# Kernel tuning notes

Hardware: AMD Instinct MI355X
Metric: run time of the kernel (lower is better)

Reference implementation:

```python
import jax, jax.numpy as jnp
import numpy as np

FP8_MAX = 448.0  # float8_e4m3fn max
NUM_HEADS = 16

def _fp8_quant_dequant(t):
    # per-(batch, head) symmetric scaling into fp8 e4m3 range, cast to fp8 and back
    amax = jnp.max(jnp.abs(t), axis=(-2, -1), keepdims=True)
    scale = FP8_MAX / jnp.maximum(amax, 1e-12)
    t8 = (t * scale).astype(jnp.float8_e4m3fn).astype(t.dtype)
    return t8 / scale

def setup_inputs() -> dict:
    key = jax.random.key(0)
    k1, k2, k3 = jax.random.split(key, 3)
    B, N, C = 2, 2048, 1024
    x = jax.random.normal(k1, (B, N, C), dtype=jnp.float32)
    w_qkv = jax.random.normal(k2, (C, 3 * C), dtype=jnp.float32) * (C ** -0.5)
    w_proj = jax.random.normal(k3, (C, C), dtype=jnp.float32) * (C ** -0.5)
    b_proj = jnp.zeros((C,), dtype=jnp.float32)
    return {"x": x, "w_qkv": w_qkv, "w_proj": w_proj, "b_proj": b_proj}

def reference(x, w_qkv, w_proj, b_proj):
    B, N, C = x.shape
    H = NUM_HEADS
    D = C // H
    scale = D ** -0.5
    qkv = (x @ w_qkv).reshape(B, N, 3, H, D).transpose(2, 0, 3, 1, 4)  # [3,B,H,N,D]
    q, k, v = qkv[0], qkv[1], qkv[2]
    # sage-style fp8 quantize/dequant of q and k fused into score computation
    q = _fp8_quant_dequant(q)
    k = _fp8_quant_dequant(k)
    scores = jnp.einsum('bhqd,bhkd->bhqk', q, k) * scale  # [B,H,N,N]
    causal = jnp.tril(jnp.ones((N, N), dtype=bool))
    scores = jnp.where(causal[None, None], scores, jnp.finfo(scores.dtype).min)
    attn = jax.nn.softmax(scores, axis=-1)
    out = jnp.einsum('bhqk,bhkd->bhqd', attn, v)  # [B,H,N,D]
    out = out.transpose(0, 2, 1, 3).reshape(B, N, C)
    return out @ w_proj + b_proj
```

## Files before the change

### kernel.cpp

```cpp
#include <hip/hip_runtime.h>

#define B_   2
#define N_   2048
#define C_   1024
#define H_   16
#define D_   64
#define BH_  (B_*H_)
#define NDH  (N_*D_)
#define M1   (B_*N_)

typedef __attribute__((ext_vector_type(4))) float    f32x4;
typedef __attribute__((ext_vector_type(8))) _Float16 f16x8;
typedef __attribute__((ext_vector_type(4))) _Float16 f16x4;
typedef __attribute__((ext_vector_type(2))) __fp16   h16x2;

#define GLOAD_LDS(gp, lp) \
  __builtin_amdgcn_global_load_lds((const __attribute__((address_space(1))) void*)(gp), \
                                   (__attribute__((address_space(3))) void*)(lp), 16, 0, 0)

__global__ void k_cvt16(const float* __restrict__ in, _Float16* __restrict__ out, int n4) {
  int i = blockIdx.x * blockDim.x + threadIdx.x;
  if (i >= n4) return;
  float4 v = ((const float4*)in)[i];
  f16x4 o;
  o.x = (_Float16)v.x; o.y = (_Float16)v.y; o.z = (_Float16)v.z; o.w = (_Float16)v.w;
  ((f16x4*)out)[i] = o;
}

__global__ __launch_bounds__(256) void k_transmerge(const float* __restrict__ wq,
                                                    const float* __restrict__ wp,
                                                    _Float16* __restrict__ whT,
                                                    _Float16* __restrict__ wpT,
                                                    unsigned* __restrict__ amax_u) {
  if (blockIdx.x == 0 && threadIdx.x < 64) amax_u[threadIdx.x] = 0u;
  __shared__ _Float16 t[64][68];
  int idx = blockIdx.x;
  const float* in; _Float16* out; int Cc, cx, cy;
  if (idx < 768) { in = wq; out = whT; Cc = 3072; cx = idx % 48; cy = idx / 48; }
  else { idx -= 768; in = wp; out = wpT; Cc = 1024; cx = idx % 16; cy = idx / 16; }
  const int R = 1024;
  int c0 = cx * 64, r0 = cy * 64;
  int tid = threadIdx.x;
  int cq = tid & 15, rq = tid >> 4;
#pragma unroll
  for (int i = 0; i < 4; ++i) {
    int r = rq + i * 16;
    float4 v = *(const float4*)(in + (size_t)(r0 + r) * Cc + c0 + cq * 4);
    t[r][cq*4+0] = (_Float16)v.x;
    t[r][cq*4+1] = (_Float16)v.y;
    t[r][cq*4+2] = (_Float16)v.z;
    t[r][cq*4+3] = (_Float16)v.w;
  }
  __syncthreads();
#pragma unroll
  for (int i = 0; i < 4; ++i) {
    int c = rq + i * 16;
    f16x4 o;
    o.x = t[cq*4+0][c];
    o.y = t[cq*4+1][c];
    o.z = t[cq*4+2][c];
    o.w = t[cq*4+3][c];
    *(f16x4*)(out + (size_t)(c0 + c) * R + r0 + cq * 4) = o;
  }
}

__global__ __launch_bounds__(256) void k_gemm_qkv(const _Float16* __restrict__ A,
                                                  const _Float16* __restrict__ BT,
                                                  _Float16* __restrict__ qh,
                                                  _Float16* __restrict__ kh,
                                                  _Float16* __restrict__ vh,
                                                  unsigned* __restrict__ amax_u) {
  __shared__ __align__(16) _Float16 As[128 * 32];
  __shared__ __align__(16) _Float16 Bs[128 * 32];
  const int tid = threadIdx.x, lane = tid & 63, wave = tid >> 6;
  const int wm = wave >> 1, wn = wave & 1;
  const int mcol = lane & 15, quad = lane >> 4;
  const int m0 = blockIdx.x * 128, n0 = blockIdx.y * 128;
  f32x4 acc[4][4] = {};
  for (int k0 = 0; k0 < 1024; k0 += 32) {
#pragma unroll
    for (int r = 0; r < 2; ++r) {
      int c = tid + r * 256;
      int row = c >> 2, kc = c & 3;
      GLOAD_LDS(A  + (size_t)(m0 + row) * 1024 + k0 + kc * 8, &As[c * 8]);
      GLOAD_LDS(BT + (size_t)(n0 + row) * 1024 + k0 + kc * 8, &Bs[c * 8]);
    }
    __syncthreads();
    f16x8 af[4], bf[4];
#pragma unroll
    for (int tm = 0; tm < 4; ++tm)
      af[tm] = *(const f16x8*)&As[(wm * 64 + tm * 16 + mcol) * 32 + quad * 8];
#pragma unroll
    for (int tn = 0; tn < 4; ++tn)
      bf[tn] = *(const f16x8*)&Bs[(wn * 64 + tn * 16 + mcol) * 32 + quad * 8];
#pragma unroll
    for (int tm = 0; tm < 4; ++tm)
#pragma unroll
      for (int tn = 0; tn < 4; ++tn)
        acc[tm][tn] = __builtin_amdgcn_mfma_f32_16x16x32_f16(af[tm], bf[tn], acc[tm][tn], 0, 0, 0);
    __syncthreads();
  }
  const int sec = n0 >> 10;
  if (sec < 2) {
    _Float16* dst = sec ? kh : qh;
    float mxv = 0.f;
#pragma unroll
    for (int tm = 0; tm < 4; ++tm)
#pragma unroll
      for (int tn = 0; tn < 4; ++tn) {
        int rowb = m0 + wm * 64 + tm * 16 + quad * 4;
        int col = n0 + wn * 64 + tn * 16 + mcol;
        int cc = col & 1023, h = cc >> 6, d = cc & 63;
        int b = rowb >> 11, n = rowb & 2047;
        f32x4 a = acc[tm][tn];
        mxv = fmaxf(mxv, fmaxf(fmaxf(fabsf(a[0]), fabsf(a[1])),
                               fmaxf(fabsf(a[2]), fabsf(a[3]))));
        f16x4 o;
        o.x = (_Float16)a[0]; o.y = (_Float16)a[1];
        o.z = (_Float16)a[2]; o.w = (_Float16)a[3];
        *(f16x4*)&dst[(size_t)(b * 16 + h) * 131072 + (size_t)(n >> 5) * 2048 + d * 32 + (n & 31)] = o;
      }
#pragma unroll
    for (int off = 32; off; off >>= 1) mxv = fmaxf(mxv, __shfl_xor(mxv, off));
    if (lane == 0) {
      int head = ((n0 & 1023) >> 6) + wn;
      int plane = (m0 >> 11) * 16 + head;
      atomicMax(&amax_u[sec * 32 + plane], __float_as_uint(mxv));
    }
  } else {
#pragma unroll
    for (int tm = 0; tm < 4; ++tm)
#pragma unroll
      for (int tn = 0; tn < 4; ++tn) {
        int rowb = m0 + wm * 64 + tm * 16 + quad * 4;
        int col = n0 + wn * 64 + tn * 16 + mcol;
        int cc = col & 1023, h = cc >> 6, d = cc & 63;
        int b = rowb >> 11, n = rowb & 2047;
        f16x4 o;
        o.x = (_Float16)acc[tm][tn][0];
        o.y = (_Float16)acc[tm][tn][1];
        o.z = (_Float16)acc[tm][tn][2];
        o.w = (_Float16)acc[tm][tn][3];
        *(f16x4*)&vh[(size_t)(b * 16 + h) * 131072 + (size_t)(n >> 5) * 2048 + d * 32 + (n & 31)] = o;
      }
  }
}

__global__ __launch_bounds__(256) void k_quant(const _Float16* __restrict__ qh,
                                               const _Float16* __restrict__ kh,
                                               const float* __restrict__ amax,
                                               char* __restrict__ q8,
                                               char* __restrict__ k8) {
  __shared__ ushort T[32][72];
  int blk = blockIdx.x;
  int which = blk >> 11;
  int idx = blk & 2047;
  int bh = idx >> 6, chunk = idx & 63;
  const _Float16* src = (which ? kh : qh) + (size_t)bh * NDH + chunk * 2048;
  float s = 448.f / fmaxf(amax[which * 32 + bh], 1e-12f);
  int t = threadIdx.x;
  f16x8 v = *(const f16x8*)(src + t * 8);
  int d = t >> 2, kk0 = (t & 3) * 8;
#pragma unroll
  for (int j = 0; j < 8; ++j) T[kk0 + j][d] = ((const ushort*)&v)[j];
  __syncthreads();
  int r = t >> 3, d0 = (t & 7) * 8;
  f16x8 row = *(const f16x8*)&T[r][d0];
  float f[8];
#pragma unroll
  for (int j = 0; j < 8; ++j) f[j] = (float)((const _Float16*)&row)[j] * s;
  int lo = 0, hi = 0;
  lo = __builtin_amdgcn_cvt_pk_fp8_f32(f[0], f[1], lo, false);
  lo = __builtin_amdgcn_cvt_pk_fp8_f32(f[2], f[3], lo, true);
  hi = __builtin_amdgcn_cvt_pk_fp8_f32(f[4], f[5], hi, false);
  hi = __builtin_amdgcn_cvt_pk_fp8_f32(f[6], f[7], hi, true);
  int2 o; o.x = lo; o.y = hi;
  if (which == 0) {
    char* dst = q8 + (size_t)bh * NDH + (size_t)(chunk * 32 + r) * 64 + d0;
    *(int2*)dst = o;
  } else {
    int e = (r >> 2) & 1;
    int mc = (r >> 3) * 4 + (r & 3);
    int kb = d0 >> 5, dq = (d0 >> 3) & 3;
    char* dst = k8 + (size_t)bh * NDH + chunk * 2048 + (e * 2 + kb) * 512 + mc * 32 + dq * 8;
    *(int2*)dst = o;
  }
}

__global__ __launch_bounds__(256, 2) void k_flash(const char* __restrict__ q8,
                                                  const char* __restrict__ k8,
                                                  const _Float16* __restrict__ vh,
                                                  const float* __restrict__ amax,
                                                  _Float16* __restrict__ attn) {
  const int bh = blockIdx.x;
  const int wave = threadIdx.x >> 6, lane = threadIdx.x & 63;
  const int mcol = lane & 15, quad = lane >> 4;
  const int slot = blockIdx.y * 4 + wave;
  const int g = 127 - slot;
  const int nt = (g >> 3) + 1;

  float sq = 448.f / fmaxf(amax[bh], 1e-12f);
  float sk = 448.f / fmaxf(amax[32 + bh], 1e-12f);
  const float c2 = (1.f / (sq * sk)) * 0.125f * 1.44269504089f;

  const size_t pbase = (size_t)bh * NDH;
  const char* kbase = k8 + pbase + mcol * 32 + quad * 8;
  const _Float16* vbase = vh + pbase + mcol * 32 + quad * 8;
  const int qrow = g * 16 + mcol;
  long aq0, aq1;
  { const char* qp = q8 + pbase + (size_t)qrow * 64;
    aq0 = *(const long*)(qp + quad * 8); aq1 = *(const long*)(qp + 32 + quad * 8); }

  f32x4 O[4] = {};
  float m_i = -3e38f, l_i = 0.f;
  const int b = bh >> 4, h = bh & 15;
  const int kq = quad * 8;

  long kc[16], kn[16];
  {
    const char* kp = kbase;
#pragma unroll
    for (int i = 0; i < 16; ++i) kc[i] = *(const long*)(kp + i * 512);
  }

  auto body = [&](int t, long (&cur)[16], long (&nxt)[16]) {
    const int n0 = t * 128;
    const bool last = (t == nt - 1);

    f32x4 s[4][2];
#pragma unroll
    for (int p = 0; p < 4; ++p)
#pragma unroll
      for (int e = 0; e < 2; ++e) {
        f32x4 z = {};
        z = __builtin_amdgcn_mfma_f32_16x16x32_fp8_fp8(cur[p * 4 + e * 2 + 0], aq0, z, 0, 0, 0);
        z = __builtin_amdgcn_mfma_f32_16x16x32_fp8_fp8(cur[p * 4 + e * 2 + 1], aq1, z, 0, 0, 0);
        s[p][e] = z;
      }
    f16x8 va[4][4];
    {
      const _Float16* vp = vbase + (size_t)(n0 >> 5) * 2048;
#pragma unroll
      for (int p = 0; p < 4; ++p)
#pragma unroll
        for (int dt = 0; dt < 4; ++dt)
          va[dt][p] = *(const f16x8*)(vp + p * 2048 + dt * 512);
    }
    if (t + 1 < nt) {
      const char* kp = kbase + (size_t)((n0 + 128) >> 5) * 2048;
#pragma unroll
      for (int i = 0; i < 16; ++i) nxt[i] = *(const long*)(kp + i * 512);
    }
    if (last) {
#pragma unroll
      for (int p = 0; p < 4; ++p)
#pragma unroll
        for (int e = 0; e < 2; ++e)
#pragma unroll
          for (int r = 0; r < 4; ++r) {
            int key = n0 + p * 32 + kq + e * 4 + r;
            s[p][e][r] = (key <= qrow) ? s[p][e][r] : -3e38f;
          }
    }
    float fm[8];
#pragma unroll
    for (int p = 0; p < 4; ++p)
#pragma unroll
      for (int e = 0; e < 2; ++e) {
        f32x4 v = s[p][e];
        fm[p * 2 + e] = fmaxf(fmaxf(v[0], v[1]), fmaxf(v[2], v[3]));
      }
    float mx = fmaxf(fmaxf(fmaxf(fm[0], fm[1]), fmaxf(fm[2], fm[3])),
                     fmaxf(fmaxf(fm[4], fm[5]), fmaxf(fm[6], fm[7])));
    mx = fmaxf(mx, m_i);
    mx = fmaxf(mx, __shfl_xor(mx, 16));
    mx = fmaxf(mx, __shfl_xor(mx, 32));
    float alpha = exp2f((m_i - mx) * c2);
    m_i = mx;
    const float nh = -mx * c2;
    float fs[8];
#pragma unroll
    for (int p = 0; p < 4; ++p)
#pragma unroll
      for (int e = 0; e < 2; ++e) {
        float p0 = exp2f(fmaf(s[p][e][0], c2, nh));
        float p1 = exp2f(fmaf(s[p][e][1], c2, nh));
        float p2 = exp2f(fmaf(s[p][e][2], c2, nh));
        float p3 = exp2f(fmaf(s[p][e][3], c2, nh));
        s[p][e][0] = p0; s[p][e][1] = p1; s[p][e][2] = p2; s[p][e][3] = p3;
        fs[p * 2 + e] = (p0 + p1) + (p2 + p3);
      }
    float sum = ((fs[0] + fs[1]) + (fs[2] + fs[3])) + ((fs[4] + fs[5]) + (fs[6] + fs[7]));
    sum += __shfl_xor(sum, 16);
    sum += __shfl_xor(sum, 32);
    l_i = l_i * alpha + sum;
#pragma unroll
    for (int dt = 0; dt < 4; ++dt)
#pragma unroll
      for (int r = 0; r < 4; ++r)
        O[dt][r] *= alpha;
#pragma unroll
    for (int p = 0; p < 4; ++p) {
      f16x8 pb;
      h16x2* pb2 = (h16x2*)&pb;
      pb2[0] = __builtin_amdgcn_cvt_pkrtz(s[p][0][0], s[p][0][1]);
      pb2[1] = __builtin_amdgcn_cvt_pkrtz(s[p][0][2], s[p][0][3]);
      pb2[2] = __builtin_amdgcn_cvt_pkrtz(s[p][1][0], s[p][1][1]);
      pb2[3] = __builtin_amdgcn_cvt_pkrtz(s[p][1][2], s[p][1][3]);
#pragma unroll
      for (int dt = 0; dt < 4; ++dt)
        O[dt] = __builtin_amdgcn_mfma_f32_16x16x32_f16(va[dt][p], pb, O[dt], 0, 0, 0);
    }
    if (last) {
      float rl = 1.f / l_i;
      _Float16* op = attn + ((size_t)b * 2048 + qrow) * 1024 + h * 64;
#pragma unroll
      for (int dt = 0; dt < 4; ++dt) {
        f16x4 o;
        o.x = (_Float16)(O[dt][0] * rl);
        o.y = (_Float16)(O[dt][1] * rl);
        o.z = (_Float16)(O[dt][2] * rl);
        o.w = (_Float16)(O[dt][3] * rl);
        *(f16x4*)(op + dt * 16 + quad * 4) = o;
      }
    }
  };

#pragma unroll 1
  for (int t = 0; t < nt; t += 2) {
    body(t, kc, kn);
    if (t + 1 < nt) body(t + 1, kn, kc);
  }
}

__global__ __launch_bounds__(256) void k_gemm_out(const _Float16* __restrict__ A,
                                                  const _Float16* __restrict__ BT,
                                                  const float* __restrict__ bias,
                                                  float* __restrict__ out) {
  __shared__ __align__(16) _Float16 As[128 * 32];
  __shared__ __align__(16) _Float16 Bs[128 * 32];
  const int tid = threadIdx.x, lane = tid & 63, wave = tid >> 6;
  const int wm = wave >> 1, wn = wave & 1;
  const int mcol = lane & 15, quad = lane >> 4;
  const int m0 = blockIdx.x * 128, n0 = blockIdx.y * 128;
  f32x4 acc[4][4] = {};
  for (int k0 = 0; k0 < 1024; k0 += 32) {
#pragma unroll
    for (int r = 0; r < 2; ++r) {
      int c = tid + r * 256;
      int row = c >> 2, kc = c & 3;
      GLOAD_LDS(A  + (size_t)(m0 + row) * 1024 + k0 + kc * 8, &As[c * 8]);
      GLOAD_LDS(BT + (size_t)(n0 + row) * 1024 + k0 + kc * 8, &Bs[c * 8]);
    }
    __syncthreads();
    f16x8 af[4], bf[4];
#pragma unroll
    for (int tm = 0; tm < 4; ++tm)
      af[tm] = *(const f16x8*)&As[(wm * 64 + tm * 16 + mcol) * 32 + quad * 8];
#pragma unroll
    for (int tn = 0; tn < 4; ++tn)
      bf[tn] = *(const f16x8*)&Bs[(wn * 64 + tn * 16 + mcol) * 32 + quad * 8];
#pragma unroll
    for (int tm = 0; tm < 4; ++tm)
#pragma unroll
      for (int tn = 0; tn < 4; ++tn)
        acc[tm][tn] = __builtin_amdgcn_mfma_f32_16x16x32_f16(af[tm], bf[tn], acc[tm][tn], 0, 0, 0);
    __syncthreads();
  }
#pragma unroll
  for (int tm = 0; tm < 4; ++tm)
#pragma unroll
    for (int tn = 0; tn < 4; ++tn)
#pragma unroll
      for (int reg = 0; reg < 4; ++reg) {
        int row = m0 + wm * 64 + tm * 16 + quad * 4 + reg;
        int col = n0 + wn * 64 + tn * 16 + mcol;
        out[(size_t)row * 1024 + col] = acc[tm][tn][reg] + bias[col];
      }
}

extern "C" void kernel_launch(void* const* d_in, const int* in_sizes, int n_in,
                              void* d_out, int out_size, void* d_ws, size_t ws_size,
                              hipStream_t stream) {
  const float* x      = (const float*)d_in[0];
  const float* w_qkv  = (const float*)d_in[1];
  const float* w_proj = (const float*)d_in[2];
  const float* b_proj = (const float*)d_in[3];
  float* out = (float*)d_out;

  char* ws = (char*)d_ws;
  _Float16* xh   = (_Float16*)ws; ws += (size_t)M1 * C_ * 2;
  _Float16* whT  = (_Float16*)ws; ws += (size_t)3 * C_ * C_ * 2;
  _Float16* wpT  = (_Float16*)ws; ws += (size_t)C_ * C_ * 2;
  _Float16* qh   = (_Float16*)ws; ws += (size_t)BH_ * NDH * 2;
  _Float16* kh   = (_Float16*)ws; ws += (size_t)BH_ * NDH * 2;
  _Float16* vh   = (_Float16*)ws; ws += (size_t)BH_ * NDH * 2;
  char*     q8   = (char*)ws;     ws += (size_t)BH_ * NDH;
  char*     k8   = (char*)ws;     ws += (size_t)BH_ * NDH;
  _Float16* attn = (_Float16*)ws; ws += (size_t)M1 * C_ * 2;
  float*    amx  = (float*)ws;    ws += 256;

  k_cvt16<<<(M1 * C_ / 4 + 255) / 256, 256, 0, stream>>>(x, xh, M1 * C_ / 4);
  k_transmerge<<<1024, 256, 0, stream>>>(w_qkv, w_proj, whT, wpT, (unsigned*)amx);
  k_gemm_qkv<<<dim3(M1 / 128, 3 * C_ / 128), 256, 0, stream>>>(xh, whT, qh, kh, vh, (unsigned*)amx);
  k_quant<<<4096, 256, 0, stream>>>(qh, kh, amx, q8, k8);
  k_flash<<<dim3(32, 32), 256, 0, stream>>>(q8, k8, vh, amx, attn);
  k_gemm_out<<<dim3(M1 / 128, C_ / 128), 256, 0, stream>>>(attn, wpT, b_proj, out);
}
```

Measured before the change: 215.1 us.

## Split flash attention key range across four waves with LDS merge of partials

Each block now owns a single 16-row query tile, and its four waves take interleaved 128-key tiles. Each wave computes its own partial softmax state (max, sum, O), then the waves merge those partials through shared memory before writing the normalised output. The goal is shorter per-wave serial chains and better load balance across the causal triangle, since the grid grows to four times as many blocks. The cost is that Q is loaded redundantly by every wave, and the change adds shared memory, a barrier and a final merge. Some waves sit idle on short rows where nt < 4.

```diff
diff --git a/kernel.cpp b/kernel.cpp
--- a/kernel.cpp
+++ b/kernel.cpp
@@ -187,17 +187,19 @@
   }
 }
 
-__global__ __launch_bounds__(256, 2) void k_flash(const char* __restrict__ q8,
-                                                  const char* __restrict__ k8,
-                                                  const _Float16* __restrict__ vh,
-                                                  const float* __restrict__ amax,
-                                                  _Float16* __restrict__ attn) {
+__global__ __launch_bounds__(256) void k_flash(const char* __restrict__ q8,
+                                               const char* __restrict__ k8,
+                                               const _Float16* __restrict__ vh,
+                                               const float* __restrict__ amax,
+                                               _Float16* __restrict__ attn) {
   const int bh = blockIdx.x;
   const int wave = threadIdx.x >> 6, lane = threadIdx.x & 63;
   const int mcol = lane & 15, quad = lane >> 4;
-  const int slot = blockIdx.y * 4 + wave;
-  const int g = 127 - slot;
+  const int g = 127 - blockIdx.y;
   const int nt = (g >> 3) + 1;
+
+  __shared__ float lds_m[4][16], lds_l[4][16];
+  __shared__ __align__(16) float lds_O[4][16][68];
 
   float sq = 448.f / fmaxf(amax[bh], 1e-12f);
   float sk = 448.f / fmaxf(amax[32 + bh], 1e-12f);
@@ -217,8 +219,8 @@
   const int kq = quad * 8;
 
   long kc[16], kn[16];
-  {
-    const char* kp = kbase;
+  if (wave < nt) {
+    const char* kp = kbase + (size_t)(wave * 4) * 2048;
 #pragma unroll
     for (int i = 0; i < 16; ++i) kc[i] = *(const long*)(kp + i * 512);
   }
@@ -246,8 +248,8 @@
         for (int dt = 0; dt < 4; ++dt)
           va[dt][p] = *(const f16x8*)(vp + p * 2048 + dt * 512);
     }
-    if (t + 1 < nt) {
-      const char* kp = kbase + (size_t)((n0 + 128) >> 5) * 2048;
+    if (t + 4 < nt) {
+      const char* kp = kbase + (size_t)((t + 4) * 4) * 2048;
 #pragma unroll
       for (int i = 0; i < 16; ++i) nxt[i] = *(const long*)(kp + i * 512);
     }
@@ -311,26 +313,39 @@
       for (int dt = 0; dt < 4; ++dt)
         O[dt] = __builtin_amdgcn_mfma_f32_16x16x32_f16(va[dt][p], pb, O[dt], 0, 0, 0);
     }
-    if (last) {
-      float rl = 1.f / l_i;
-      _Float16* op = attn + ((size_t)b * 2048 + qrow) * 1024 + h * 64;
-#pragma unroll
-      for (int dt = 0; dt < 4; ++dt) {
-        f16x4 o;
-        o.x = (_Float16)(O[dt][0] * rl);
-        o.y = (_Float16)(O[dt][1] * rl);
-        o.z = (_Float16)(O[dt][2] * rl);
-        o.w = (_Float16)(O[dt][3] * rl);
-        *(f16x4*)(op + dt * 16 + quad * 4) = o;
-      }
-    }
   };
 
 #pragma unroll 1
-  for (int t = 0; t < nt; t += 2) {
+  for (int t = wave; t < nt; t += 8) {
     body(t, kc, kn);
-    if (t + 1 < nt) body(t + 1, kn, kc);
-  }
+    if (t + 4 < nt) body(t + 4, kn, kc);
+  }
+
+  if (quad == 0) { lds_m[wave][mcol] = m_i; lds_l[wave][mcol] = l_i; }
+#pragma unroll
+  for (int dt = 0; dt < 4; ++dt)
+    *(f32x4*)&lds_O[wave][mcol][dt * 16 + quad * 4] = O[dt];
+  __syncthreads();
+
+  float m0 = lds_m[0][mcol], m1 = lds_m[1][mcol];
+  float m2 = lds_m[2][mcol], m3 = lds_m[3][mcol];
+  float mm = fmaxf(fmaxf(m0, m1), fmaxf(m2, m3));
+  float f0 = exp2f((m0 - mm) * c2), f1 = exp2f((m1 - mm) * c2);
+  float f2 = exp2f((m2 - mm) * c2), f3 = exp2f((m3 - mm) * c2);
+  float l = lds_l[0][mcol] * f0 + lds_l[1][mcol] * f1 +
+            lds_l[2][mcol] * f2 + lds_l[3][mcol] * f3;
+  f32x4 o0 = *(const f32x4*)&lds_O[0][mcol][wave * 16 + quad * 4];
+  f32x4 o1 = *(const f32x4*)&lds_O[1][mcol][wave * 16 + quad * 4];
+  f32x4 o2 = *(const f32x4*)&lds_O[2][mcol][wave * 16 + quad * 4];
+  f32x4 o3 = *(const f32x4*)&lds_O[3][mcol][wave * 16 + quad * 4];
+  float rl = 1.f / l;
+  _Float16* op = attn + ((size_t)b * 2048 + qrow) * 1024 + h * 64 + wave * 16 + quad * 4;
+  f16x4 o;
+  o.x = (_Float16)((o0[0] * f0 + o1[0] * f1 + o2[0] * f2 + o3[0] * f3) * rl);
+  o.y = (_Float16)((o0[1] * f0 + o1[1] * f1 + o2[1] * f2 + o3[1] * f3) * rl);
+  o.z = (_Float16)((o0[2] * f0 + o1[2] * f1 + o2[2] * f2 + o3[2] * f3) * rl);
+  o.w = (_Float16)((o0[3] * f0 + o1[3] * f1 + o2[3] * f2 + o3[3] * f3) * rl);
+  *(f16x4*)op = o;
 }
 
 __global__ __launch_bounds__(256) void k_gemm_out(const _Float16* __restrict__ A,
@@ -404,6 +419,6 @@
   k_transmerge<<<1024, 256, 0, stream>>>(w_qkv, w_proj, whT, wpT, (unsigned*)amx);
   k_gemm_qkv<<<dim3(M1 / 128, 3 * C_ / 128), 256, 0, stream>>>(xh, whT, qh, kh, vh, (unsigned*)amx);
   k_quant<<<4096, 256, 0, stream>>>(qh, kh, amx, q8, k8);
-  k_flash<<<dim3(32, 32), 256, 0, stream>>>(q8, k8, vh, amx, attn);
+  k_flash<<<dim3(32, 128), 256, 0, stream>>>(q8, k8, vh, amx, attn);
   k_gemm_out<<<dim3(M1 / 128, C_ / 128), 256, 0, stream>>>(attn, wpT, b_proj, out);
 }
```

Measured after the change: 253.5 us. +17.9%, slower.

## Share K/V tiles across waves via LDS in flash attention kernel

Applied to the files above, without the earlier changes.

Each block now stages the 128-key K (fp8) and V (fp16) tile into shared memory with global_load_lds, and all four waves read operands from LDS instead of loading K and V independently from global memory. This cuts redundant global/L2 traffic, since previously each wave fetched the same K/V tiles. In exchange the loop is no longer software-pipelined (no register double-buffering of K), adds two barriers per tile, and waves with shorter causal ranges idle through the block's maximum tile count. The occupancy hint of 2 blocks per CU was also dropped from launch bounds.

```diff
diff --git a/kernel.cpp b/kernel.cpp
--- a/kernel.cpp
+++ b/kernel.cpp
@@ -187,25 +187,29 @@
   }
 }
 
-__global__ __launch_bounds__(256, 2) void k_flash(const char* __restrict__ q8,
-                                                  const char* __restrict__ k8,
-                                                  const _Float16* __restrict__ vh,
-                                                  const float* __restrict__ amax,
-                                                  _Float16* __restrict__ attn) {
+__global__ __launch_bounds__(256) void k_flash(const char* __restrict__ q8,
+                                               const char* __restrict__ k8,
+                                               const _Float16* __restrict__ vh,
+                                               const float* __restrict__ amax,
+                                               _Float16* __restrict__ attn) {
   const int bh = blockIdx.x;
-  const int wave = threadIdx.x >> 6, lane = threadIdx.x & 63;
+  const int tid = threadIdx.x;
+  const int wave = tid >> 6, lane = tid & 63;
   const int mcol = lane & 15, quad = lane >> 4;
-  const int slot = blockIdx.y * 4 + wave;
-  const int g = 127 - slot;
+  const int g = 127 - (blockIdx.y * 4 + wave);
   const int nt = (g >> 3) + 1;
+  const int ntmax = ((127 - blockIdx.y * 4) >> 3) + 1;
+
+  __shared__ __align__(16) char     Ks[8192];
+  __shared__ __align__(16) _Float16 Vs[8192];
 
   float sq = 448.f / fmaxf(amax[bh], 1e-12f);
   float sk = 448.f / fmaxf(amax[32 + bh], 1e-12f);
   const float c2 = (1.f / (sq * sk)) * 0.125f * 1.44269504089f;
 
   const size_t pbase = (size_t)bh * NDH;
-  const char* kbase = k8 + pbase + mcol * 32 + quad * 8;
-  const _Float16* vbase = vh + pbase + mcol * 32 + quad * 8;
+  const char* kpl = k8 + pbase;
+  const _Float16* vpl = vh + pbase;
   const int qrow = g * 16 + mcol;
   long aq0, aq1;
   { const char* qp = q8 + pbase + (size_t)qrow * 64;
@@ -215,121 +219,113 @@
   float m_i = -3e38f, l_i = 0.f;
   const int b = bh >> 4, h = bh & 15;
   const int kq = quad * 8;
-
-  long kc[16], kn[16];
-  {
-    const char* kp = kbase;
-#pragma unroll
-    for (int i = 0; i < 16; ++i) kc[i] = *(const long*)(kp + i * 512);
-  }
-
-  auto body = [&](int t, long (&cur)[16], long (&nxt)[16]) {
-    const int n0 = t * 128;
-    const bool last = (t == nt - 1);
-
-    f32x4 s[4][2];
-#pragma unroll
-    for (int p = 0; p < 4; ++p)
-#pragma unroll
-      for (int e = 0; e < 2; ++e) {
-        f32x4 z = {};
-        z = __builtin_amdgcn_mfma_f32_16x16x32_fp8_fp8(cur[p * 4 + e * 2 + 0], aq0, z, 0, 0, 0);
-        z = __builtin_amdgcn_mfma_f32_16x16x32_fp8_fp8(cur[p * 4 + e * 2 + 1], aq1, z, 0, 0, 0);
-        s[p][e] = z;
+  const int koff = mcol * 32 + quad * 8;
+  const int voff = mcol * 32 + quad * 8;
+
+#pragma unroll 1
+  for (int t = 0; t < ntmax; ++t) {
+    {
+      const char* ks = kpl + (size_t)t * 8192;
+      const _Float16* vs = vpl + (size_t)t * 8192;
+#pragma unroll
+      for (int r = 0; r < 2; ++r)
+        GLOAD_LDS(ks + (tid + r * 256) * 16, &Ks[(tid + r * 256) * 16]);
+#pragma unroll
+      for (int r = 0; r < 4; ++r)
+        GLOAD_LDS(vs + (tid + r * 256) * 8, &Vs[(tid + r * 256) * 8]);
+    }
+    __syncthreads();
+
+    if (t < nt) {
+      const int n0 = t * 128;
+      f32x4 s[4][2];
+#pragma unroll
+      for (int p = 0; p < 4; ++p)
+#pragma unroll
+        for (int e = 0; e < 2; ++e) {
+          long ka = *(const long*)&Ks[(p * 4 + e * 2 + 0) * 512 + koff];
+          long kb = *(const long*)&Ks[(p * 4 + e * 2 + 1) * 512 + koff];
+          f32x4 z = {};
+          z = __builtin_amdgcn_mfma_f32_16x16x32_fp8_fp8(ka, aq0, z, 0, 0, 0);
+          z = __builtin_amdgcn_mfma_f32_16x16x32_fp8_fp8(kb, aq1, z, 0, 0, 0);
+          s[p][e] = z;
+        }
+      if (t >= nt - 1) {
+#pragma unroll
+        for (int p = 0; p < 4; ++p)
+#pragma unroll
+          for (int e = 0; e < 2; ++e)
+#pragma unroll
+            for (int r = 0; r < 4; ++r) {
+              int key = n0 + p * 32 + kq + e * 4 + r;
+              s[p][e][r] = (key <= qrow) ? s[p][e][r] : -3e38f;
+            }
       }
-    f16x8 va[4][4];
-    {
-      const _Float16* vp = vbase + (size_t)(n0 >> 5) * 2048;
+      float fm[8];
 #pragma unroll
       for (int p = 0; p < 4; ++p)
 #pragma unroll
-        for (int dt = 0; dt < 4; ++dt)
-          va[dt][p] = *(const f16x8*)(vp + p * 2048 + dt * 512);
-    }
-    if (t + 1 < nt) {
-      const char* kp = kbase + (size_t)((n0 + 128) >> 5) * 2048;
-#pragma unroll
-      for (int i = 0; i < 16; ++i) nxt[i] = *(const long*)(kp + i * 512);
-    }
-    if (last) {
+        for (int e = 0; e < 2; ++e) {
+          f32x4 v = s[p][e];
+          fm[p * 2 + e] = fmaxf(fmaxf(v[0], v[1]), fmaxf(v[2], v[3]));
+        }
+      float mx = fmaxf(fmaxf(fmaxf(fm[0], fm[1]), fmaxf(fm[2], fm[3])),
+                       fmaxf(fmaxf(fm[4], fm[5]), fmaxf(fm[6], fm[7])));
+      mx = fmaxf(mx, m_i);
+      mx = fmaxf(mx, __shfl_xor(mx, 16));
+      mx = fmaxf(mx, __shfl_xor(mx, 32));
+      float alpha = exp2f((m_i - mx) * c2);
+      m_i = mx;
+      const float nh = -mx * c2;
+      float fs[8];
 #pragma unroll
       for (int p = 0; p < 4; ++p)
 #pragma unroll
-        for (int e = 0; e < 2; ++e)
-#pragma unroll
-          for (int r = 0; r < 4; ++r) {
-            int key = n0 + p * 32 + kq + e * 4 + r;
-            s[p][e][r] = (key <= qrow) ? s[p][e][r] : -3e38f;
-          }
-    }
-    float fm[8];
-#pragma unroll
-    for (int p = 0; p < 4; ++p)
-#pragma unroll
-      for (int e = 0; e < 2; ++e) {
-        f32x4 v = s[p][e];
-        fm[p * 2 + e] = fmaxf(fmaxf(v[0], v[1]), fmaxf(v[2], v[3]));
-      }
-    float mx = fmaxf(fmaxf(fmaxf(fm[0], fm[1]), fmaxf(fm[2], fm[3])),
-                     fmaxf(fmaxf(fm[4], fm[5]), fmaxf(fm[6], fm[7])));
-    mx = fmaxf(mx, m_i);
-    mx = fmaxf(mx, __shfl_xor(mx, 16));
-    mx = fmaxf(mx, __shfl_xor(mx, 32));
-    float alpha = exp2f((m_i - mx) * c2);
-    m_i = mx;
-    const float nh = -mx * c2;
-    float fs[8];
-#pragma unroll
-    for (int p = 0; p < 4; ++p)
-#pragma unroll
-      for (int e = 0; e < 2; ++e) {
-        float p0 = exp2f(fmaf(s[p][e][0], c2, nh));
-        float p1 = exp2f(fmaf(s[p][e][1], c2, nh));
-        float p2 = exp2f(fmaf(s[p][e][2], c2, nh));
-        float p3 = exp2f(fmaf(s[p][e][3], c2, nh));
-        s[p][e][0] = p0; s[p][e][1] = p1; s[p][e][2] = p2; s[p][e][3] = p3;
-        fs[p * 2 + e] = (p0 + p1) + (p2 + p3);
-      }
-    float sum = ((fs[0] + fs[1]) + (fs[2] + fs[3])) + ((fs[4] + fs[5]) + (fs[6] + fs[7]));
-    sum += __shfl_xor(sum, 16);
-    sum += __shfl_xor(sum, 32);
-    l_i = l_i * alpha + sum;
-#pragma unroll
-    for (int dt = 0; dt < 4; ++dt)
-#pragma unroll
-      for (int r = 0; r < 4; ++r)
-        O[dt][r] *= alpha;
-#pragma unroll
-    for (int p = 0; p < 4; ++p) {
-      f16x8 pb;
-      h16x2* pb2 = (h16x2*)&pb;
-      pb2[0] = __builtin_amdgcn_cvt_pkrtz(s[p][0][0], s[p][0][1]);
-      pb2[1] = __builtin_amdgcn_cvt_pkrtz(s[p][0][2], s[p][0][3]);
-      pb2[2] = __builtin_amdgcn_cvt_pkrtz(s[p][1][0], s[p][1][1]);
-      pb2[3] = __builtin_amdgcn_cvt_pkrtz(s[p][1][2], s[p][1][3]);
+        for (int e = 0; e < 2; ++e) {
+          float p0 = exp2f(fmaf(s[p][e][0], c2, nh));
+          float p1 = exp2f(fmaf(s[p][e][1], c2, nh));
+          float p2 = exp2f(fmaf(s[p][e][2], c2, nh));
+          float p3 = exp2f(fmaf(s[p][e][3], c2, nh));
+          s[p][e][0] = p0; s[p][e][1] = p1; s[p][e][2] = p2; s[p][e][3] = p3;
+          fs[p * 2 + e] = (p0 + p1) + (p2 + p3);
+        }
+      float sum = ((fs[0] + fs[1]) + (fs[2] + fs[3])) + ((fs[4] + fs[5]) + (fs[6] + fs[7]));
+      sum += __shfl_xor(sum, 16);
+      sum += __shfl_xor(sum, 32);
+      l_i = l_i * alpha + sum;
 #pragma unroll
       for (int dt = 0; dt < 4; ++dt)
-        O[dt] = __builtin_amdgcn_mfma_f32_16x16x32_f16(va[dt][p], pb, O[dt], 0, 0, 0);
-    }
-    if (last) {
-      float rl = 1.f / l_i;
-      _Float16* op = attn + ((size_t)b * 2048 + qrow) * 1024 + h * 64;
-#pragma unroll
-      for (int dt = 0; dt < 4; ++dt) {
-        f16x4 o;
-        o.x = (_Float16)(O[dt][0] * rl);
-        o.y = (_Float16)(O[dt][1] * rl);
-        o.z = (_Float16)(O[dt][2] * rl);
-        o.w = (_Float16)(O[dt][3] * rl);
-        *(f16x4*)(op + dt * 16 + quad * 4) = o;
+#pragma unroll
+        for (int r = 0; r < 4; ++r)
+          O[dt][r] *= alpha;
+#pragma unroll
+      for (int p = 0; p < 4; ++p) {
+        f16x8 pb;
+        h16x2* pb2 = (h16x2*)&pb;
+        pb2[0] = __builtin_amdgcn_cvt_pkrtz(s[p][0][0], s[p][0][1]);
+        pb2[1] = __builtin_amdgcn_cvt_pkrtz(s[p][0][2], s[p][0][3]);
+        pb2[2] = __builtin_amdgcn_cvt_pkrtz(s[p][1][0], s[p][1][1]);
+        pb2[3] = __builtin_amdgcn_cvt_pkrtz(s[p][1][2], s[p][1][3]);
+#pragma unroll
+        for (int dt = 0; dt < 4; ++dt) {
+          f16x8 va = *(const f16x8*)&Vs[p * 2048 + dt * 512 + voff];
+          O[dt] = __builtin_amdgcn_mfma_f32_16x16x32_f16(va, pb, O[dt], 0, 0, 0);
+        }
       }
     }
-  };
-
-#pragma unroll 1
-  for (int t = 0; t < nt; t += 2) {
-    body(t, kc, kn);
-    if (t + 1 < nt) body(t + 1, kn, kc);
+    __syncthreads();
+  }
+
+  float rl = 1.f / l_i;
+  _Float16* op = attn + ((size_t)b * 2048 + qrow) * 1024 + h * 64;
+#pragma unroll
+  for (int dt = 0; dt < 4; ++dt) {
+    f16x4 o;
+    o.x = (_Float16)(O[dt][0] * rl);
+    o.y = (_Float16)(O[dt][1] * rl);
+    o.z = (_Float16)(O[dt][2] * rl);
+    o.w = (_Float16)(O[dt][3] * rl);
+    *(f16x4*)(op + dt * 16 + quad * 4) = o;
   }
 }
 
```

After: 209.0 us. -2.8%, faster.
